# Optimization experiments

Hardware: AMD Instinct MI355X
Metric: run time of the kernel (lower is better)

## Reference

```python
import jax, jax.numpy as jnp
import numpy as np
import math

N, E = 50000, 500000
T, R, H, NH, L, DIN, MAXT = 3, 4, 8, 128, 2, 166, 240
DK = NH // H


def _sinusoid_table():
    pos = np.arange(MAXT)[:, None].astype(np.float64)
    div = np.exp(np.arange(0, NH, 2) * -(math.log(10000.0) / NH))
    tab = np.zeros((MAXT, NH), np.float32)
    tab[:, 0::2] = np.sin(pos * div) / math.sqrt(NH)
    tab[:, 1::2] = np.cos(pos * div) / math.sqrt(NH)
    return jnp.asarray(tab)

RTE_TAB = _sinusoid_table()  # fixed (non-trainable) sinusoid embedding, as in pyHGT RTE


def _per_type_linear(x, t_idx, W, b):
    # W: [T, din, dout]; dispatch linear by node/edge type (T is small)
    out = jnp.zeros((x.shape[0], W.shape[-1]), x.dtype)
    for t in range(W.shape[0]):
        out = jnp.where((t_idx == t)[:, None], x @ W[t] + b[t], out)
    return out


def _hgt_layer(x, node_type, src, tgt, edge_type, edge_time,
               kW, kb, qW, qb, vW, vb, aW, ab,
               rel_att, rel_msg, rel_pri, skip, rteW, rteb):
    n = x.shape[0]
    # target-type query at node level
    q = _per_type_linear(x, node_type, qW, qb).reshape(n, H, DK)
    # RTE: source features + Linear(sinusoid_emb(edge_time)), per edge
    src_vec = x[src] + RTE_TAB[edge_time] @ rteW + rteb          # [E, NH]
    s_type = node_type[src]
    k = _per_type_linear(src_vec, s_type, kW, kb).reshape(-1, H, DK)
    v = _per_type_linear(src_vec, s_type, vW, vb).reshape(-1, H, DK)
    # relation-specific transforms, dispatched by edge type (R is small)
    k_rel = jnp.zeros_like(k)
    v_rel = jnp.zeros_like(v)
    for r in range(R):
        m = (edge_type == r)[:, None, None]
        k_rel = jnp.where(m, jnp.einsum('ehd,hdf->ehf', k, rel_att[r]), k_rel)
        v_rel = jnp.where(m, jnp.einsum('ehd,hdf->ehf', v, rel_msg[r]), v_rel)
    att = (q[tgt] * k_rel).sum(-1) * rel_pri[edge_type] / math.sqrt(DK)  # [E, H]
    # segment softmax over incoming edges of each target node
    amax = jax.lax.stop_gradient(jax.ops.segment_max(att, tgt, num_segments=n))
    ex = jnp.exp(att - amax[tgt])
    den = jax.ops.segment_sum(ex, tgt, num_segments=n)
    w = ex / jnp.maximum(den[tgt], 1e-9)
    agg = jax.ops.segment_sum((v_rel * w[..., None]).reshape(-1, NH), tgt, num_segments=n)
    trans = _per_type_linear(jax.nn.gelu(agg, approximate=False), node_type, aW, ab)
    alpha = jax.nn.sigmoid(skip)[node_type][:, None]  # per-target-type learned skip
    return trans * alpha + x * (1.0 - alpha)


def reference(node_feature, node_type, edge_time, edge_index, edge_type,
              adapt_W, adapt_b, kW, kb, qW, qb, vW, vb, aW, ab,
              rel_att, rel_msg, rel_pri, skip, rteW, rteb):
    # per-type adapter: gather -> linear -> tanh -> scatter-back
    h = jnp.tanh(_per_type_linear(node_feature, node_type, adapt_W, adapt_b))
    src, tgt = edge_index[0], edge_index[1]
    for l in range(L):
        h = _hgt_layer(h, node_type, src, tgt, edge_type, edge_time,
                       kW[l], kb[l], qW[l], qb[l], vW[l], vb[l], aW[l], ab[l],
                       rel_att[l], rel_msg[l], rel_pri[l], skip[l], rteW[l], rteb[l])
    return h


def setup_inputs() -> dict:
    key = jax.random.key(0)
    ks = jax.random.split(key, 16)
    s_in = 1.0 / math.sqrt(DIN)
    s_h = 1.0 / math.sqrt(NH)
    eye = jnp.tile(jnp.eye(DK, dtype=jnp.float32), (L, R, H, 1, 1))
    return {
        'node_feature': jax.random.normal(ks[0], (N, DIN), jnp.float32),
        'node_type': jax.random.randint(ks[1], (N,), 0, T),
        'edge_time': jax.random.randint(ks[2], (E,), 0, MAXT),
        'edge_index': jax.random.randint(ks[3], (2, E), 0, N),
        'edge_type': jax.random.randint(ks[4], (E,), 0, R),
        'adapt_W': jax.random.normal(ks[5], (T, DIN, NH), jnp.float32) * s_in,
        'adapt_b': jnp.zeros((T, NH), jnp.float32),
        'kW': jax.random.normal(ks[6], (L, T, NH, NH), jnp.float32) * s_h,
        'kb': jnp.zeros((L, T, NH), jnp.float32),
        'qW': jax.random.normal(ks[7], (L, T, NH, NH), jnp.float32) * s_h,
        'qb': jnp.zeros((L, T, NH), jnp.float32),
        'vW': jax.random.normal(ks[8], (L, T, NH, NH), jnp.float32) * s_h,
        'vb': jnp.zeros((L, T, NH), jnp.float32),
        'aW': jax.random.normal(ks[9], (L, T, NH, NH), jnp.float32) * s_h,
        'ab': jnp.zeros((L, T, NH), jnp.float32),
        'rel_att': eye + jax.random.normal(ks[10], (L, R, H, DK, DK), jnp.float32) * 0.02,
        'rel_msg': eye + jax.random.normal(ks[11], (L, R, H, DK, DK), jnp.float32) * 0.02,
        'rel_pri': jnp.ones((L, R, H), jnp.float32),
        'skip': jnp.ones((L, T), jnp.float32),
        'rteW': jax.random.normal(ks[12], (L, NH, NH), jnp.float32) * s_h,
        'rteb': jnp.zeros((L, NH), jnp.float32),
    }
```

## Files before the change

### kernel.cpp

```cpp
#include <hip/hip_runtime.h>
#include <hip/hip_fp16.h>
#include <float.h>
#include <math.h>

#define N_NODES 50000
#define N_EDGES 500000
#define TT 3
#define RR 4
#define HH 8
#define NHID 128
#define NLAYER 2
#define DIN_ 166
#define MAXT_ 240
#define DKH 16
#define NPB 16
#define NPB2 32


__global__ void k_sin_table(float* __restrict__ tab) {
    int idx = blockIdx.x * blockDim.x + threadIdx.x;
    if (idx >= MAXT_ * 64) return;
    int p = idx / 64, i2 = idx % 64;
    const double c = -9.210340371976184 / 128.0;
    double div = exp((double)(2 * i2) * c);
    double a = (double)p * div;
    const double s128 = 0.08838834764831845;
    tab[p * NHID + 2 * i2]     = (float)(sin(a) * s128);
    tab[p * NHID + 2 * i2 + 1] = (float)(cos(a) * s128);
}

__global__ void k_bin(const int* __restrict__ ntype, int* __restrict__ cnt,
                      int* __restrict__ lists) {
    int n = blockIdx.x * 256 + threadIdx.x;
    int t = (n < N_NODES) ? ntype[n] : -1;
    int lane = threadIdx.x & 63;
    #pragma unroll
    for (int tt = 0; tt < TT; ++tt) {
        unsigned long long mask = __ballot(t == tt);
        if (mask) {
            int leader = (int)__ffsll(mask) - 1;
            int base = 0;
            if (lane == leader) base = atomicAdd(&cnt[tt], __popcll(mask));
            base = __shfl(base, leader);
            if (t == tt) {
                int rank = __popcll(mask & ((1ULL << lane) - 1ULL));
                lists[tt * N_NODES + base + rank] = n;
            }
        }
    }
}


__global__ void k_deg(const int* __restrict__ tgt, int* __restrict__ deg) {
    int e = blockIdx.x * 256 + threadIdx.x;
    if (e < N_EDGES) atomicAdd(&deg[tgt[e]], 1);
}

__global__ void k_scan(const int* __restrict__ deg, int* __restrict__ rowptr) {
    __shared__ int wsum[16];
    __shared__ int carry_s;
    int tid = threadIdx.x;
    int lane = tid & 63, wid = tid >> 6;
    if (tid == 0) { carry_s = 0; rowptr[0] = 0; }
    __syncthreads();
    for (int base = 0; base < N_NODES; base += 1024) {
        int idx = base + tid;
        int x = (idx < N_NODES) ? deg[idx] : 0;
        #pragma unroll
        for (int off = 1; off < 64; off <<= 1) {
            int y = __shfl_up(x, off, 64);
            if (lane >= off) x += y;
        }
        if (lane == 63) wsum[wid] = x;
        __syncthreads();
        if (wid == 0) {
            int w = (lane < 16) ? wsum[lane] : 0;
            #pragma unroll
            for (int off = 1; off < 16; off <<= 1) {
                int y = __shfl_up(w, off, 64);
                if (lane >= off) w += y;
            }
            if (lane < 16) wsum[lane] = w;
        }
        __syncthreads();
        int waveoff = (wid > 0) ? wsum[wid - 1] : 0;
        int incl = carry_s + waveoff + x;
        if (idx < N_NODES) rowptr[idx + 1] = incl;
        __syncthreads();
        if (tid == 1023) carry_s = incl;
        __syncthreads();
    }
}

__global__ void k_fill(const int* __restrict__ src, const int* __restrict__ tgt,
                       const int* __restrict__ etype, const int* __restrict__ etime,
                       const int* __restrict__ ntype, int* __restrict__ cursor,
                       int* __restrict__ sE, int* __restrict__ attr,
                       int* __restrict__ gE) {
    int e = blockIdx.x * 256 + threadIdx.x;
    if (e >= N_EDGES) return;
    int g = tgt[e];
    int s = src[e];
    int r = etype[e];
    int tm = etime[e];
    int t = ntype[s];
    int p = atomicAdd(&cursor[g], 1);
    sE[p] = s;
    attr[p] = (r << 12) | (tm * TT + t);
    gE[p] = g;
}


__global__ void k_adapter(const float* __restrict__ x, const int* __restrict__ cnt,
                          const int* __restrict__ lists,
                          const float* __restrict__ W, const float* __restrict__ b,
                          float* __restrict__ h) {
    int t = blockIdx.y;
    int c = cnt[t];
    int i0 = blockIdx.x * NPB;
    if (i0 >= c) return;
    int j = threadIdx.x;
    __shared__ float xs[NPB][DIN_];
    __shared__ int nidx[NPB];
    if (j < NPB) nidx[j] = (i0 + j < c) ? lists[t * N_NODES + i0 + j] : -1;
    __syncthreads();
    int nr[NPB];
    #pragma unroll
    for (int m = 0; m < NPB; ++m) nr[m] = nidx[m];
    #pragma unroll
    for (int m = 0; m < NPB; ++m) {
        int n = nr[m];
        for (int d = j; d < DIN_; d += 128)
            xs[m][d] = (n >= 0) ? x[(size_t)n * DIN_ + d] : 0.f;
    }
    __syncthreads();
    const float* Wt = W + (size_t)t * DIN_ * NHID;
    float bj = b[t * NHID + j];
    float acc[NPB];
    #pragma unroll
    for (int m = 0; m < NPB; ++m) acc[m] = bj;
    for (int d = 0; d < DIN_; ++d) {
        float w = Wt[d * NHID + j];
        #pragma unroll
        for (int m = 0; m < NPB; ++m) acc[m] = fmaf(xs[m][d], w, acc[m]);
    }
    #pragma unroll
    for (int m = 0; m < NPB; ++m) {
        int n = nr[m];
        if (n >= 0) h[(size_t)n * NHID + j] = tanhf(acc[m]);
    }
}

__global__ __launch_bounds__(128) void k_node_lin(
        const float* __restrict__ h, const int* __restrict__ cnt,
        const int* __restrict__ lists,
        const float* __restrict__ Wk, const float* __restrict__ bk,
        const float* __restrict__ Wq, const float* __restrict__ bq,
        const float* __restrict__ Wv, const float* __restrict__ bv,
        const float* __restrict__ rel_att,
        __half* __restrict__ hk16, __half* __restrict__ hv16,
        float* __restrict__ u3f) {
    int t = blockIdx.y;
    int c = cnt[t];
    int i0 = blockIdx.x * NPB2;
    if (i0 >= c) return;
    int j = threadIdx.x;
    __shared__ int nidx[NPB2];
    __shared__ float hsT[NHID][36];
    float (*aqs)[132] = (float(*)[132])&hsT[0][0];

    if (j < NPB2) nidx[j] = (i0 + j < c) ? lists[t * N_NODES + i0 + j] : -1;
    __syncthreads();
    for (int m = 0; m < NPB2; ++m) {
        int n = nidx[m];
        hsT[j][m] = (n >= 0) ? h[(size_t)n * NHID + j] : 0.f;
    }
    __syncthreads();

    const float* WkT = Wk + (size_t)t * NHID * NHID;
    const float* WqT = Wq + (size_t)t * NHID * NHID;
    const float* WvT = Wv + (size_t)t * NHID * NHID;
    float ak[NPB2], aq[NPB2], av[NPB2];
    float bkj = bk[t * NHID + j], bqj = bq[t * NHID + j], bvj = bv[t * NHID + j];
    #pragma unroll
    for (int m = 0; m < NPB2; ++m) { ak[m] = bkj; aq[m] = bqj; av[m] = bvj; }
    for (int i = 0; i < NHID; ++i) {
        float wk = WkT[i * NHID + j];
        float wq = WqT[i * NHID + j];
        float wv = WvT[i * NHID + j];
        const float4* hrow = (const float4*)&hsT[i][0];
        #pragma unroll
        for (int cc = 0; cc < 8; ++cc) {
            float4 h4 = hrow[cc];
            int mb = cc * 4;
            ak[mb+0] = fmaf(h4.x, wk, ak[mb+0]);
            ak[mb+1] = fmaf(h4.y, wk, ak[mb+1]);
            ak[mb+2] = fmaf(h4.z, wk, ak[mb+2]);
            ak[mb+3] = fmaf(h4.w, wk, ak[mb+3]);
            aq[mb+0] = fmaf(h4.x, wq, aq[mb+0]);
            aq[mb+1] = fmaf(h4.y, wq, aq[mb+1]);
            aq[mb+2] = fmaf(h4.z, wq, aq[mb+2]);
            aq[mb+3] = fmaf(h4.w, wq, aq[mb+3]);
            av[mb+0] = fmaf(h4.x, wv, av[mb+0]);
            av[mb+1] = fmaf(h4.y, wv, av[mb+1]);
            av[mb+2] = fmaf(h4.z, wv, av[mb+2]);
            av[mb+3] = fmaf(h4.w, wv, av[mb+3]);
        }
    }
    #pragma unroll
    for (int m = 0; m < NPB2; ++m) {
        int n = nidx[m];
        if (n >= 0) {
            hk16[(size_t)n * NHID + j] = __float2half(ak[m]);
            hv16[(size_t)n * NHID + j] = __float2half(av[m]);
        }
    }
    __syncthreads();
    for (int m = 0; m < NPB2; ++m) aqs[m][j] = aq[m];
    __syncthreads();

    int hh = j >> 4, f = j & 15;
    float A[RR][DKH];
    #pragma unroll
    for (int r = 0; r < RR; ++r) {
        const float4* Arow = (const float4*)(rel_att + (((r * HH + hh) << 8) | (f * 16)));
        #pragma unroll
        for (int cc = 0; cc < 4; ++cc) {
            float4 a4 = Arow[cc];
            A[r][cc*4+0] = a4.x; A[r][cc*4+1] = a4.y;
            A[r][cc*4+2] = a4.z; A[r][cc*4+3] = a4.w;
        }
    }
    for (int m = 0; m < NPB2; ++m) {
        int n = nidx[m];
        if (n < 0) continue;
        const float4* arow = (const float4*)&aqs[m][hh * 16];
        float qv[DKH];
        #pragma unroll
        for (int cc = 0; cc < 4; ++cc) {
            float4 q4 = arow[cc];
            qv[cc*4+0] = q4.x; qv[cc*4+1] = q4.y;
            qv[cc*4+2] = q4.z; qv[cc*4+3] = q4.w;
        }
        #pragma unroll
        for (int r = 0; r < RR; ++r) {
            float u = 0.f;
            #pragma unroll
            for (int d = 0; d < DKH; ++d) u = fmaf(A[r][d], qv[d], u);
            u3f[((size_t)n * RR + r) * NHID + j] = u;
        }
    }
}

__global__ __launch_bounds__(128) void k_out(
        const float* __restrict__ agg, const float* __restrict__ hin,
        const int* __restrict__ cnt, const int* __restrict__ lists,
        const float* __restrict__ aW, const float* __restrict__ ab,
        const float* __restrict__ skp, float* __restrict__ hout) {
    int t = blockIdx.y;
    int c = cnt[t];
    int i0 = blockIdx.x * NPB2;
    if (i0 >= c) return;
    int j = threadIdx.x;
    __shared__ int nidx[NPB2];
    __shared__ float gsT[NHID][36];
    if (j < NPB2) nidx[j] = (i0 + j < c) ? lists[t * N_NODES + i0 + j] : -1;
    __syncthreads();
    for (int m = 0; m < NPB2; ++m) {
        int n = nidx[m];
        float xv = (n >= 0) ? agg[(size_t)n * NHID + j] : 0.f;
        gsT[j][m] = 0.5f * xv * (1.f + erff(xv * 0.7071067811865476f));
    }
    __syncthreads();
    const float* Wt = aW + (size_t)t * NHID * NHID;
    float bj = ab[t * NHID + j];
    float acc[NPB2];
    #pragma unroll
    for (int m = 0; m < NPB2; ++m) acc[m] = bj;
    for (int i = 0; i < NHID; ++i) {
        float w = Wt[i * NHID + j];
        const float4* grow = (const float4*)&gsT[i][0];
        #pragma unroll
        for (int cc = 0; cc < 8; ++cc) {
            float4 g4 = grow[cc];
            int mb = cc * 4;
            acc[mb+0] = fmaf(g4.x, w, acc[mb+0]);
            acc[mb+1] = fmaf(g4.y, w, acc[mb+1]);
            acc[mb+2] = fmaf(g4.z, w, acc[mb+2]);
            acc[mb+3] = fmaf(g4.w, w, acc[mb+3]);
        }
    }
    float alpha = 1.f / (1.f + expf(-skp[t]));
    #pragma unroll
    for (int m = 0; m < NPB2; ++m) {
        int n = nidx[m];
        if (n >= 0)
            hout[(size_t)n * NHID + j] =
                acc[m] * alpha + hin[(size_t)n * NHID + j] * (1.f - alpha);
    }
}


__global__ void k_rte_proj(const float* __restrict__ tab, const float* __restrict__ rteW,
                           const float* __restrict__ rteb, float* __restrict__ proj) {
    int p = blockIdx.x;
    int j = threadIdx.x;
    __shared__ float ts[NHID];
    ts[j] = tab[p * NHID + j];
    __syncthreads();
    float acc = rteb[j];
    for (int i = 0; i < NHID; ++i) acc = fmaf(ts[i], rteW[i * NHID + j], acc);
    proj[p * NHID + j] = acc;
}

__global__ void k_rkv(const float* __restrict__ proj, const float* __restrict__ kW,
                      const float* __restrict__ vW, __half* __restrict__ RK16,
                      float* __restrict__ RV) {
    int p = blockIdx.x, t = blockIdx.y;
    int j = threadIdx.x;
    __shared__ float ps[NHID];
    ps[j] = proj[p * NHID + j];
    __syncthreads();
    const float* Wk = kW + (size_t)t * NHID * NHID;
    const float* Wv = vW + (size_t)t * NHID * NHID;
    float ak = 0.f, av = 0.f;
    for (int i = 0; i < NHID; ++i) {
        float pi = ps[i];
        ak = fmaf(pi, Wk[i * NHID + j], ak);
        av = fmaf(pi, Wv[i * NHID + j], av);
    }
    RK16[((size_t)p * TT + t) * NHID + j] = __float2half(ak);
    RV[((size_t)p * TT + t) * NHID + j] = av;
}


__global__ __launch_bounds__(256) void k_att(
        const __half* __restrict__ hk16, const float* __restrict__ u3f,
        const __half* __restrict__ RK16,
        const int* __restrict__ sE, const int* __restrict__ attr,
        const int* __restrict__ gE,
        const float* __restrict__ rel_pri, float* __restrict__ att2) {
    int idx = blockIdx.x * 256 + threadIdx.x;
    if (idx >= N_EDGES * HH) return;
    int k = idx >> 3, h = idx & 7;
    int s = sE[k];
    int a = attr[k];
    int r = a >> 12, row = a & 4095;
    int g = gE[k];
    const __half2* hk2 = (const __half2*)hk16 + (size_t)s * 64 + h * 8;
    const __half2* rk2 = (const __half2*)RK16 + (size_t)row * 64 + h * 8;
    const float4* u4 = (const float4*)(u3f + ((size_t)g * RR + r) * NHID) + h * 4;
    float acc = 0.f;
    #pragma unroll
    for (int i2 = 0; i2 < 4; ++i2) {
        float4 u = u4[i2];
        float2 p0 = __half22float2(hk2[2 * i2]);
        float2 r0 = __half22float2(rk2[2 * i2]);
        float2 p1 = __half22float2(hk2[2 * i2 + 1]);
        float2 r1 = __half22float2(rk2[2 * i2 + 1]);
        acc = fmaf(p0.x + r0.x, u.x, acc);
        acc = fmaf(p0.y + r0.y, u.y, acc);
        acc = fmaf(p1.x + r1.x, u.z, acc);
        acc = fmaf(p1.y + r1.y, u.w, acc);
    }
    acc *= rel_pri[r * HH + h] * 0.25f;
    att2[(size_t)h * N_EDGES + k] = acc;
}


__global__ __launch_bounds__(128) void k_csr(
        const __half* __restrict__ hv16, const float* __restrict__ RV,
        float* __restrict__ att2,
        const int* __restrict__ rowptr, const int* __restrict__ sE,
        const int* __restrict__ attr,
        const float* __restrict__ rel_msg, float* __restrict__ agg) {
    int n = blockIdx.x;
    int tid = threadIdx.x;
    int h = tid >> 4, f = tid & 15;
    int beg = rowptr[n], end = rowptr[n + 1];
    float* ap = att2 + (size_t)h * N_EDGES;

    float m = -FLT_MAX;
    for (int k = beg + f; k < end; k += 16) m = fmaxf(m, ap[k]);
    #pragma unroll
    for (int mask = 1; mask <= 8; mask <<= 1)
        m = fmaxf(m, __shfl_xor(m, mask, 64));

    float ssum = 0.f;
    for (int k = beg + f; k < end; k += 16) {
        float ex = expf(ap[k] - m);
        ap[k] = ex;
        ssum += ex;
    }
    #pragma unroll
    for (int mask = 1; mask <= 8; mask <<= 1)
        ssum += __shfl_xor(ssum, mask, 64);
    float rden = 1.f / fmaxf(ssum, 1e-9f);
    __syncthreads();

    float a0 = 0.f, a1 = 0.f, a2 = 0.f, a3 = 0.f;
    #pragma unroll 2
    for (int k = beg; k < end; ++k) {
        int s = sE[k];
        int a = attr[k];
        int r = a >> 12, row = a & 4095;
        float vvt = __half2float(hv16[(size_t)s * NHID + tid])
                    + RV[(size_t)row * NHID + tid];
        float wv = ap[k] * vvt;
        a0 += (r == 0) ? wv : 0.f;
        a1 += (r == 1) ? wv : 0.f;
        a2 += (r == 2) ? wv : 0.f;
        a3 += (r == 3) ? wv : 0.f;
    }

    int lanebase = tid & 48;
    float out = 0.f;
    #pragma unroll
    for (int r = 0; r < RR; ++r) {
        float ar = (r == 0) ? a0 : (r == 1) ? a1 : (r == 2) ? a2 : a3;
        const float* M = rel_msg + ((r * HH + h) << 8) + f;
        #pragma unroll
        for (int d = 0; d < DKH; ++d) {
            float vd = __shfl(ar, lanebase + d, 64);
            out = fmaf(vd, M[d * 16], out);
        }
    }
    agg[(size_t)n * NHID + tid] = out * rden;
}


extern "C" void kernel_launch(void* const* d_in, const int* in_sizes, int n_in,
                              void* d_out, int out_size, void* d_ws, size_t ws_size,
                              hipStream_t stream) {
    const float* node_feature = (const float*)d_in[0];
    const int*   node_type    = (const int*)d_in[1];
    const int*   edge_time    = (const int*)d_in[2];
    const int*   edge_index   = (const int*)d_in[3];
    const int*   edge_type    = (const int*)d_in[4];
    const float* adapt_W = (const float*)d_in[5];
    const float* adapt_b = (const float*)d_in[6];
    const float* kW = (const float*)d_in[7];
    const float* kb = (const float*)d_in[8];
    const float* qW = (const float*)d_in[9];
    const float* qb = (const float*)d_in[10];
    const float* vW = (const float*)d_in[11];
    const float* vb = (const float*)d_in[12];
    const float* aW = (const float*)d_in[13];
    const float* ab = (const float*)d_in[14];
    const float* rel_att = (const float*)d_in[15];
    const float* rel_msg = (const float*)d_in[16];
    const float* rel_pri = (const float*)d_in[17];
    const float* skip = (const float*)d_in[18];
    const float* rteW = (const float*)d_in[19];
    const float* rteb = (const float*)d_in[20];

    const int* src = edge_index;
    const int* tgt = edge_index + N_EDGES;

    float* ws = (float*)d_ws;
    float* hA   = ws; ws += (size_t)N_NODES * NHID;
    float* agg  = ws; ws += (size_t)N_NODES * NHID;
    float* att2 = ws; ws += (size_t)N_EDGES * HH;
    float* u3f  = ws; ws += (size_t)N_NODES * RR * NHID;
    float* tab  = ws; ws += MAXT_ * NHID;
    float* proj = ws; ws += MAXT_ * NHID;
    float* RV   = ws; ws += MAXT_ * TT * NHID;
    __half* hk16 = (__half*)ws; ws += (size_t)N_NODES * NHID / 2;
    __half* hv16 = (__half*)ws; ws += (size_t)N_NODES * NHID / 2;
    __half* RK16 = (__half*)ws; ws += (size_t)MAXT_ * TT * NHID / 2;
    int*   deg    = (int*)ws; ws += N_NODES;
    int*   rowptr = (int*)ws; ws += N_NODES + 1;
    int*   cursor = (int*)ws; ws += N_NODES;
    int*   sE     = (int*)ws; ws += N_EDGES;
    int*   attr   = (int*)ws; ws += N_EDGES;
    int*   gE     = (int*)ws; ws += N_EDGES;
    int*   cnt    = (int*)ws; ws += 4;
    int*   lists  = (int*)ws; ws += (size_t)TT * N_NODES;

    const int nodeBlocksX = (N_NODES + NPB - 1) / NPB;
    const int nodeBlocksX2 = (N_NODES + NPB2 - 1) / NPB2;
    dim3 nodeGrid(nodeBlocksX, TT);
    dim3 nodeGrid2(nodeBlocksX2, TT);
    const int eB = (N_EDGES + 255) / 256;
    const int edgeBlocks = (N_EDGES * HH + 255) / 256;

    hipMemsetAsync(cnt, 0, 4 * sizeof(int), stream);
    hipMemsetAsync(deg, 0, N_NODES * sizeof(int), stream);
    k_bin<<<(N_NODES + 255) / 256, 256, 0, stream>>>(node_type, cnt, lists);
    k_deg<<<eB, 256, 0, stream>>>(tgt, deg);
    k_scan<<<1, 1024, 0, stream>>>(deg, rowptr);
    hipMemcpyAsync(cursor, rowptr, N_NODES * sizeof(int),
                   hipMemcpyDeviceToDevice, stream);
    k_fill<<<eB, 256, 0, stream>>>(src, tgt, edge_type, edge_time, node_type,
                                   cursor, sE, attr, gE);

    k_sin_table<<<(MAXT_ * 64 + 255) / 256, 256, 0, stream>>>(tab);
    k_adapter<<<nodeGrid, 128, 0, stream>>>(node_feature, cnt, lists, adapt_W, adapt_b, hA);

    for (int l = 0; l < NLAYER; ++l) {
        const float* hin = hA;
        float* hout = (l == 0) ? hA : (float*)d_out;
        const float* kW_l = kW + (size_t)l * TT * NHID * NHID;
        const float* kb_l = kb + (size_t)l * TT * NHID;
        const float* qW_l = qW + (size_t)l * TT * NHID * NHID;
        const float* qb_l = qb + (size_t)l * TT * NHID;
        const float* vW_l = vW + (size_t)l * TT * NHID * NHID;
        const float* vb_l = vb + (size_t)l * TT * NHID;
        const float* aW_l = aW + (size_t)l * TT * NHID * NHID;
        const float* ab_l = ab + (size_t)l * TT * NHID;
        const float* ratt_l = rel_att + (size_t)l * RR * HH * DKH * DKH;
        const float* rmsg_l = rel_msg + (size_t)l * RR * HH * DKH * DKH;
        const float* rpri_l = rel_pri + (size_t)l * RR * HH;
        const float* skip_l = skip + (size_t)l * TT;
        const float* rteW_l = rteW + (size_t)l * NHID * NHID;
        const float* rteb_l = rteb + (size_t)l * NHID;

        k_rte_proj<<<MAXT_, 128, 0, stream>>>(tab, rteW_l, rteb_l, proj);
        dim3 rkvGrid(MAXT_, TT);
        k_rkv<<<rkvGrid, 128, 0, stream>>>(proj, kW_l, vW_l, RK16, RV);
        k_node_lin<<<nodeGrid2, 128, 0, stream>>>(hin, cnt, lists,
                                                  kW_l, kb_l, qW_l, qb_l, vW_l, vb_l,
                                                  ratt_l, hk16, hv16, u3f);
        k_att<<<edgeBlocks, 256, 0, stream>>>(hk16, u3f, RK16, sE, attr, gE,
                                              rpri_l, att2);
        k_csr<<<N_NODES, 128, 0, stream>>>(hv16, RV, att2, rowptr, sE, attr,
                                           rmsg_l, agg);
        k_out<<<nodeGrid2, 128, 0, stream>>>(agg, hin, cnt, lists, aW_l, ab_l,
                                             skip_l, hout);
    }
}
```

Baseline: 1.028 ms.

## Parallelize CSR scan, fuse RTE projection, widen edge work, store agg in fp16

Replaces the single-block serial prefix scan over node degrees with a three-kernel multi-block scan. Fuses the RTE projection into the k/v relative-table kernel so the separate launch and intermediate buffer go away, at the cost of recomputing the projection once per node type. The attention kernel now handles two edges per thread with vectorized index loads and float2 stores, and the CSR aggregation loop is manually unrolled by four to expose more memory-level parallelism. The aggregated features are stored as fp16 to halve that traffic, which adds rounding error ahead of the GELU and output linear.

```diff
diff --git a/kernel.cpp b/kernel.cpp
--- a/kernel.cpp
+++ b/kernel.cpp
@@ -56,40 +56,59 @@
     if (e < N_EDGES) atomicAdd(&deg[tgt[e]], 1);
 }
 
-__global__ void k_scan(const int* __restrict__ deg, int* __restrict__ rowptr) {
-    __shared__ int wsum[16];
-    __shared__ int carry_s;
-    int tid = threadIdx.x;
-    int lane = tid & 63, wid = tid >> 6;
-    if (tid == 0) { carry_s = 0; rowptr[0] = 0; }
-    __syncthreads();
-    for (int base = 0; base < N_NODES; base += 1024) {
-        int idx = base + tid;
-        int x = (idx < N_NODES) ? deg[idx] : 0;
-        #pragma unroll
-        for (int off = 1; off < 64; off <<= 1) {
-            int y = __shfl_up(x, off, 64);
-            if (lane >= off) x += y;
-        }
-        if (lane == 63) wsum[wid] = x;
-        __syncthreads();
-        if (wid == 0) {
-            int w = (lane < 16) ? wsum[lane] : 0;
-            #pragma unroll
-            for (int off = 1; off < 16; off <<= 1) {
-                int y = __shfl_up(w, off, 64);
-                if (lane >= off) w += y;
-            }
-            if (lane < 16) wsum[lane] = w;
-        }
-        __syncthreads();
-        int waveoff = (wid > 0) ? wsum[wid - 1] : 0;
-        int incl = carry_s + waveoff + x;
-        if (idx < N_NODES) rowptr[idx + 1] = incl;
-        __syncthreads();
-        if (tid == 1023) carry_s = incl;
-        __syncthreads();
-    }
+__global__ void k_scan1(const int* __restrict__ deg, int* __restrict__ rowptr,
+                        int* __restrict__ bsum) {
+    int b = blockIdx.x, t = threadIdx.x;
+    int idx = b * 256 + t;
+    int x = (idx < N_NODES) ? deg[idx] : 0;
+    int lane = t & 63, wid = t >> 6;
+    __shared__ int wsum[4];
+    #pragma unroll
+    for (int off = 1; off < 64; off <<= 1) {
+        int y = __shfl_up(x, off, 64);
+        if (lane >= off) x += y;
+    }
+    if (lane == 63) wsum[wid] = x;
+    __syncthreads();
+    if (t == 0) {
+        int acc = 0;
+        #pragma unroll
+        for (int i = 0; i < 4; ++i) { int v = wsum[i]; wsum[i] = acc; acc += v; }
+        bsum[b] = acc;
+    }
+    __syncthreads();
+    x += wsum[wid];
+    if (idx < N_NODES) rowptr[idx + 1] = x;
+}
+
+__global__ void k_scan2(int* __restrict__ bsum, int nb) {
+    int t = threadIdx.x;
+    int orig = (t < nb) ? bsum[t] : 0;
+    int x = orig;
+    int lane = t & 63, wid = t >> 6;
+    __shared__ int wsum[4];
+    #pragma unroll
+    for (int off = 1; off < 64; off <<= 1) {
+        int y = __shfl_up(x, off, 64);
+        if (lane >= off) x += y;
+    }
+    if (lane == 63) wsum[wid] = x;
+    __syncthreads();
+    if (t == 0) {
+        int acc = 0;
+        #pragma unroll
+        for (int i = 0; i < 4; ++i) { int v = wsum[i]; wsum[i] = acc; acc += v; }
+    }
+    __syncthreads();
+    x += wsum[wid];
+    if (t < nb) bsum[t] = x - orig;
+}
+
+__global__ void k_scan3(int* __restrict__ rowptr, const int* __restrict__ bsum) {
+    int b = blockIdx.x, t = threadIdx.x;
+    int idx = b * 256 + t;
+    if (idx < N_NODES) rowptr[idx + 1] += bsum[b];
+    if (idx == 0) rowptr[0] = 0;
 }
 
 __global__ void k_fill(const int* __restrict__ src, const int* __restrict__ tgt,
@@ -253,7 +272,7 @@
 }
 
 __global__ __launch_bounds__(128) void k_out(
-        const float* __restrict__ agg, const float* __restrict__ hin,
+        const __half* __restrict__ agg16, const float* __restrict__ hin,
         const int* __restrict__ cnt, const int* __restrict__ lists,
         const float* __restrict__ aW, const float* __restrict__ ab,
         const float* __restrict__ skp, float* __restrict__ hout) {
@@ -268,7 +287,7 @@
     __syncthreads();
     for (int m = 0; m < NPB2; ++m) {
         int n = nidx[m];
-        float xv = (n >= 0) ? agg[(size_t)n * NHID + j] : 0.f;
+        float xv = (n >= 0) ? __half2float(agg16[(size_t)n * NHID + j]) : 0.f;
         gsT[j][m] = 0.5f * xv * (1.f + erff(xv * 0.7071067811865476f));
     }
     __syncthreads();
@@ -301,25 +320,19 @@
 }
 
 
-__global__ void k_rte_proj(const float* __restrict__ tab, const float* __restrict__ rteW,
-                           const float* __restrict__ rteb, float* __restrict__ proj) {
-    int p = blockIdx.x;
+__global__ void k_rkv(const float* __restrict__ tab, const float* __restrict__ rteW,
+                      const float* __restrict__ rteb,
+                      const float* __restrict__ kW, const float* __restrict__ vW,
+                      __half* __restrict__ RK16, float* __restrict__ RV) {
+    int p = blockIdx.x, t = blockIdx.y;
     int j = threadIdx.x;
     __shared__ float ts[NHID];
+    __shared__ float ps[NHID];
     ts[j] = tab[p * NHID + j];
     __syncthreads();
-    float acc = rteb[j];
-    for (int i = 0; i < NHID; ++i) acc = fmaf(ts[i], rteW[i * NHID + j], acc);
-    proj[p * NHID + j] = acc;
-}
-
-__global__ void k_rkv(const float* __restrict__ proj, const float* __restrict__ kW,
-                      const float* __restrict__ vW, __half* __restrict__ RK16,
-                      float* __restrict__ RV) {
-    int p = blockIdx.x, t = blockIdx.y;
-    int j = threadIdx.x;
-    __shared__ float ps[NHID];
-    ps[j] = proj[p * NHID + j];
+    float pj = rteb[j];
+    for (int i = 0; i < NHID; ++i) pj = fmaf(ts[i], rteW[i * NHID + j], pj);
+    ps[j] = pj;
     __syncthreads();
     const float* Wk = kW + (size_t)t * NHID * NHID;
     const float* Wv = vW + (size_t)t * NHID * NHID;
@@ -341,30 +354,45 @@
         const int* __restrict__ gE,
         const float* __restrict__ rel_pri, float* __restrict__ att2) {
     int idx = blockIdx.x * 256 + threadIdx.x;
-    if (idx >= N_EDGES * HH) return;
-    int k = idx >> 3, h = idx & 7;
-    int s = sE[k];
-    int a = attr[k];
-    int r = a >> 12, row = a & 4095;
-    int g = gE[k];
-    const __half2* hk2 = (const __half2*)hk16 + (size_t)s * 64 + h * 8;
-    const __half2* rk2 = (const __half2*)RK16 + (size_t)row * 64 + h * 8;
-    const float4* u4 = (const float4*)(u3f + ((size_t)g * RR + r) * NHID) + h * 4;
-    float acc = 0.f;
+    if (idx >= (N_EDGES / 2) * HH) return;
+    int p = idx >> 3, h = idx & 7;
+    int k0 = p * 2;
+    int2 ss = *(const int2*)(sE + k0);
+    int2 aa = *(const int2*)(attr + k0);
+    int2 gg = *(const int2*)(gE + k0);
+    int r0 = aa.x >> 12, row0 = aa.x & 4095;
+    int r1 = aa.y >> 12, row1 = aa.y & 4095;
+    const __half2* hkA = (const __half2*)hk16 + (size_t)ss.x * 64 + h * 8;
+    const __half2* rkA = (const __half2*)RK16 + (size_t)row0 * 64 + h * 8;
+    const float4*  uA  = (const float4*)(u3f + ((size_t)gg.x * RR + r0) * NHID) + h * 4;
+    const __half2* hkB = (const __half2*)hk16 + (size_t)ss.y * 64 + h * 8;
+    const __half2* rkB = (const __half2*)RK16 + (size_t)row1 * 64 + h * 8;
+    const float4*  uB  = (const float4*)(u3f + ((size_t)gg.y * RR + r1) * NHID) + h * 4;
+    float accA = 0.f, accB = 0.f;
     #pragma unroll
     for (int i2 = 0; i2 < 4; ++i2) {
-        float4 u = u4[i2];
-        float2 p0 = __half22float2(hk2[2 * i2]);
-        float2 r0 = __half22float2(rk2[2 * i2]);
-        float2 p1 = __half22float2(hk2[2 * i2 + 1]);
-        float2 r1 = __half22float2(rk2[2 * i2 + 1]);
-        acc = fmaf(p0.x + r0.x, u.x, acc);
-        acc = fmaf(p0.y + r0.y, u.y, acc);
-        acc = fmaf(p1.x + r1.x, u.z, acc);
-        acc = fmaf(p1.y + r1.y, u.w, acc);
-    }
-    acc *= rel_pri[r * HH + h] * 0.25f;
-    att2[(size_t)h * N_EDGES + k] = acc;
+        float4 ua = uA[i2];
+        float2 pa0 = __half22float2(hkA[2*i2]);
+        float2 ra0 = __half22float2(rkA[2*i2]);
+        float2 pa1 = __half22float2(hkA[2*i2+1]);
+        float2 ra1 = __half22float2(rkA[2*i2+1]);
+        accA = fmaf(pa0.x + ra0.x, ua.x, accA);
+        accA = fmaf(pa0.y + ra0.y, ua.y, accA);
+        accA = fmaf(pa1.x + ra1.x, ua.z, accA);
+        accA = fmaf(pa1.y + ra1.y, ua.w, accA);
+        float4 ub = uB[i2];
+        float2 pb0 = __half22float2(hkB[2*i2]);
+        float2 rb0 = __half22float2(rkB[2*i2]);
+        float2 pb1 = __half22float2(hkB[2*i2+1]);
+        float2 rb1 = __half22float2(rkB[2*i2+1]);
+        accB = fmaf(pb0.x + rb0.x, ub.x, accB);
+        accB = fmaf(pb0.y + rb0.y, ub.y, accB);
+        accB = fmaf(pb1.x + rb1.x, ub.z, accB);
+        accB = fmaf(pb1.y + rb1.y, ub.w, accB);
+    }
+    accA *= rel_pri[r0 * HH + h] * 0.25f;
+    accB *= rel_pri[r1 * HH + h] * 0.25f;
+    *(float2*)(att2 + (size_t)h * N_EDGES + k0) = make_float2(accA, accB);
 }
 
 
@@ -373,7 +401,7 @@
         float* __restrict__ att2,
         const int* __restrict__ rowptr, const int* __restrict__ sE,
         const int* __restrict__ attr,
-        const float* __restrict__ rel_msg, float* __restrict__ agg) {
+        const float* __restrict__ rel_msg, __half* __restrict__ agg16) {
     int n = blockIdx.x;
     int tid = threadIdx.x;
     int h = tid >> 4, f = tid & 15;
@@ -399,14 +427,33 @@
     __syncthreads();
 
     float a0 = 0.f, a1 = 0.f, a2 = 0.f, a3 = 0.f;
-    #pragma unroll 2
-    for (int k = beg; k < end; ++k) {
+    int k = beg;
+    for (; k + 4 <= end; k += 4) {
+        int s0 = sE[k],   s1 = sE[k+1], s2 = sE[k+2], s3 = sE[k+3];
+        int t0 = attr[k], t1 = attr[k+1], t2 = attr[k+2], t3 = attr[k+3];
+        float w0 = ap[k], w1 = ap[k+1], w2 = ap[k+2], w3 = ap[k+3];
+        float v0 = __half2float(hv16[(size_t)s0 * NHID + tid]) + RV[(size_t)(t0 & 4095) * NHID + tid];
+        float v1 = __half2float(hv16[(size_t)s1 * NHID + tid]) + RV[(size_t)(t1 & 4095) * NHID + tid];
+        float v2 = __half2float(hv16[(size_t)s2 * NHID + tid]) + RV[(size_t)(t2 & 4095) * NHID + tid];
+        float v3 = __half2float(hv16[(size_t)s3 * NHID + tid]) + RV[(size_t)(t3 & 4095) * NHID + tid];
+        float wv0 = w0 * v0, wv1 = w1 * v1, wv2 = w2 * v2, wv3 = w3 * v3;
+        int r0 = t0 >> 12, r1 = t1 >> 12, r2 = t2 >> 12, r3 = t3 >> 12;
+        a0 += ((r0 == 0) ? wv0 : 0.f) + ((r1 == 0) ? wv1 : 0.f)
+            + ((r2 == 0) ? wv2 : 0.f) + ((r3 == 0) ? wv3 : 0.f);
+        a1 += ((r0 == 1) ? wv0 : 0.f) + ((r1 == 1) ? wv1 : 0.f)
+            + ((r2 == 1) ? wv2 : 0.f) + ((r3 == 1) ? wv3 : 0.f);
+        a2 += ((r0 == 2) ? wv0 : 0.f) + ((r1 == 2) ? wv1 : 0.f)
+            + ((r2 == 2) ? wv2 : 0.f) + ((r3 == 2) ? wv3 : 0.f);
+        a3 += ((r0 == 3) ? wv0 : 0.f) + ((r1 == 3) ? wv1 : 0.f)
+            + ((r2 == 3) ? wv2 : 0.f) + ((r3 == 3) ? wv3 : 0.f);
+    }
+    for (; k < end; ++k) {
         int s = sE[k];
         int a = attr[k];
-        int r = a >> 12, row = a & 4095;
         float vvt = __half2float(hv16[(size_t)s * NHID + tid])
-                    + RV[(size_t)row * NHID + tid];
+                    + RV[(size_t)(a & 4095) * NHID + tid];
         float wv = ap[k] * vvt;
+        int r = a >> 12;
         a0 += (r == 0) ? wv : 0.f;
         a1 += (r == 1) ? wv : 0.f;
         a2 += (r == 2) ? wv : 0.f;
@@ -425,7 +472,7 @@
             out = fmaf(vd, M[d * 16], out);
         }
     }
-    agg[(size_t)n * NHID + tid] = out * rden;
+    agg16[(size_t)n * NHID + tid] = __float2half(out * rden);
 }
 
 
@@ -459,21 +506,21 @@
 
     float* ws = (float*)d_ws;
     float* hA   = ws; ws += (size_t)N_NODES * NHID;
-    float* agg  = ws; ws += (size_t)N_NODES * NHID;
     float* att2 = ws; ws += (size_t)N_EDGES * HH;
     float* u3f  = ws; ws += (size_t)N_NODES * RR * NHID;
     float* tab  = ws; ws += MAXT_ * NHID;
-    float* proj = ws; ws += MAXT_ * NHID;
     float* RV   = ws; ws += MAXT_ * TT * NHID;
-    __half* hk16 = (__half*)ws; ws += (size_t)N_NODES * NHID / 2;
-    __half* hv16 = (__half*)ws; ws += (size_t)N_NODES * NHID / 2;
-    __half* RK16 = (__half*)ws; ws += (size_t)MAXT_ * TT * NHID / 2;
+    __half* agg16 = (__half*)ws; ws += (size_t)N_NODES * NHID / 2;
+    __half* hk16  = (__half*)ws; ws += (size_t)N_NODES * NHID / 2;
+    __half* hv16  = (__half*)ws; ws += (size_t)N_NODES * NHID / 2;
+    __half* RK16  = (__half*)ws; ws += (size_t)MAXT_ * TT * NHID / 2;
     int*   deg    = (int*)ws; ws += N_NODES;
-    int*   rowptr = (int*)ws; ws += N_NODES + 1;
+    int*   rowptr = (int*)ws; ws += N_NODES + 2;
     int*   cursor = (int*)ws; ws += N_NODES;
     int*   sE     = (int*)ws; ws += N_EDGES;
     int*   attr   = (int*)ws; ws += N_EDGES;
     int*   gE     = (int*)ws; ws += N_EDGES;
+    int*   bsum   = (int*)ws; ws += 256;
     int*   cnt    = (int*)ws; ws += 4;
     int*   lists  = (int*)ws; ws += (size_t)TT * N_NODES;
 
@@ -482,13 +529,16 @@
     dim3 nodeGrid(nodeBlocksX, TT);
     dim3 nodeGrid2(nodeBlocksX2, TT);
     const int eB = (N_EDGES + 255) / 256;
-    const int edgeBlocks = (N_EDGES * HH + 255) / 256;
+    const int attBlocks = ((N_EDGES / 2) * HH + 255) / 256;
+    const int scanBlocks = (N_NODES + 255) / 256;
 
     hipMemsetAsync(cnt, 0, 4 * sizeof(int), stream);
     hipMemsetAsync(deg, 0, N_NODES * sizeof(int), stream);
     k_bin<<<(N_NODES + 255) / 256, 256, 0, stream>>>(node_type, cnt, lists);
     k_deg<<<eB, 256, 0, stream>>>(tgt, deg);
-    k_scan<<<1, 1024, 0, stream>>>(deg, rowptr);
+    k_scan1<<<scanBlocks, 256, 0, stream>>>(deg, rowptr, bsum);
+    k_scan2<<<1, 256, 0, stream>>>(bsum, scanBlocks);
+    k_scan3<<<scanBlocks, 256, 0, stream>>>(rowptr, bsum);
     hipMemcpyAsync(cursor, rowptr, N_NODES * sizeof(int),
                    hipMemcpyDeviceToDevice, stream);
     k_fill<<<eB, 256, 0, stream>>>(src, tgt, edge_type, edge_time, node_type,
@@ -515,17 +565,16 @@
         const float* rteW_l = rteW + (size_t)l * NHID * NHID;
         const float* rteb_l = rteb + (size_t)l * NHID;
 
-        k_rte_proj<<<MAXT_, 128, 0, stream>>>(tab, rteW_l, rteb_l, proj);
         dim3 rkvGrid(MAXT_, TT);
-        k_rkv<<<rkvGrid, 128, 0, stream>>>(proj, kW_l, vW_l, RK16, RV);
+        k_rkv<<<rkvGrid, 128, 0, stream>>>(tab, rteW_l, rteb_l, kW_l, vW_l, RK16, RV);
         k_node_lin<<<nodeGrid2, 128, 0, stream>>>(hin, cnt, lists,
                                                   kW_l, kb_l, qW_l, qb_l, vW_l, vb_l,
                                                   ratt_l, hk16, hv16, u3f);
-        k_att<<<edgeBlocks, 256, 0, stream>>>(hk16, u3f, RK16, sE, attr, gE,
-                                              rpri_l, att2);
+        k_att<<<attBlocks, 256, 0, stream>>>(hk16, u3f, RK16, sE, attr, gE,
+                                             rpri_l, att2);
         k_csr<<<N_NODES, 128, 0, stream>>>(hv16, RV, att2, rowptr, sE, attr,
-                                           rmsg_l, agg);
-        k_out<<<nodeGrid2, 128, 0, stream>>>(agg, hin, cnt, lists, aW_l, ab_l,
+                                           rmsg_l, agg16);
+        k_out<<<nodeGrid2, 128, 0, stream>>>(agg16, hin, cnt, lists, aW_l, ab_l,
                                              skip_l, hout);
     }
 }
```

Result: faster. 920.9 us (-10.5%).
